# Optimization experiments

Measured on AMD Instinct MI355X. Metric: run time of the kernel, lower is better.

The kernel has to match this reference:

```python
import jax, jax.numpy as jnp
import numpy as np

H = 96          # hidden_dim / GatedGraphConv out_channels
L = 6           # num_layers
F_IN = 32       # num_node_features
G = 4096        # number of graphs in batch
BN_EPS = 1e-5


def setup_inputs() -> dict:
    key = jax.random.key(0)
    ks = jax.random.split(key, 16)
    N, E = 100000, 400000
    x = jax.random.normal(ks[0], (N, F_IN), dtype=jnp.float32)
    edge_index = jax.random.randint(ks[1], (2, E), 0, N, dtype=jnp.int64)
    batch = jnp.sort(jax.random.randint(ks[2], (N,), 0, G, dtype=jnp.int64))
    s = 1.0 / np.sqrt(H)
    conv_w = jax.random.uniform(ks[3], (L, H, H), jnp.float32, -s, s)
    w_ih = jax.random.uniform(ks[4], (3 * H, H), jnp.float32, -s, s)
    w_hh = jax.random.uniform(ks[5], (3 * H, H), jnp.float32, -s, s)
    b_ih = jax.random.uniform(ks[6], (3 * H,), jnp.float32, -s, s)
    b_hh = jax.random.uniform(ks[7], (3 * H,), jnp.float32, -s, s)
    bn_gamma = jnp.ones((H,), jnp.float32)
    bn_beta = jnp.zeros((H,), jnp.float32)
    s1 = 1.0 / np.sqrt(H)
    fc1_w = jax.random.uniform(ks[8], (4 * H, H), jnp.float32, -s1, s1)
    fc1_b = jax.random.uniform(ks[9], (4 * H,), jnp.float32, -s1, s1)
    s2 = 1.0 / np.sqrt(4 * H)
    fc2_w = jax.random.uniform(ks[10], (H, 4 * H), jnp.float32, -s2, s2)
    fc2_b = jax.random.uniform(ks[11], (H,), jnp.float32, -s2, s2)
    fc3_w = jax.random.uniform(ks[12], (1, H), jnp.float32, -s1, s1)
    fc3_b = jax.random.uniform(ks[13], (1,), jnp.float32, -s1, s1)
    return dict(x=x, edge_index=edge_index, batch=batch, conv_w=conv_w,
                w_ih=w_ih, w_hh=w_hh, b_ih=b_ih, b_hh=b_hh,
                bn_gamma=bn_gamma, bn_beta=bn_beta,
                fc1_w=fc1_w, fc1_b=fc1_b, fc2_w=fc2_w, fc2_b=fc2_b,
                fc3_w=fc3_w, fc3_b=fc3_b)


def _gated_graph_conv(x, src, dst, conv_w, w_ih, w_hh, b_ih, b_hh):
    N = x.shape[0]
    # PyG zero-pads input features up to out_channels
    h = jnp.pad(x, ((0, 0), (0, H - x.shape[1])))
    for i in range(L):
        m = h @ conv_w[i]                         # [N, H]
        agg = jnp.zeros((N, H), m.dtype).at[dst].add(m[src])  # scatter-add at targets
        gi = agg @ w_ih.T + b_ih                  # [N, 3H]
        gh = h @ w_hh.T + b_hh                    # [N, 3H]
        i_r, i_z, i_n = jnp.split(gi, 3, axis=-1)
        h_r, h_z, h_n = jnp.split(gh, 3, axis=-1)
        r = jax.nn.sigmoid(i_r + h_r)
        z = jax.nn.sigmoid(i_z + h_z)
        n = jnp.tanh(i_n + r * h_n)
        h = (1.0 - z) * n + z * h
    return h


def reference(x, edge_index, batch, conv_w, w_ih, w_hh, b_ih, b_hh,
              bn_gamma, bn_beta, fc1_w, fc1_b, fc2_w, fc2_b, fc3_w, fc3_b):
    src, dst = edge_index[0], edge_index[1]
    h = _gated_graph_conv(x, src, dst, conv_w, w_ih, w_hh, b_ih, b_hh)
    h = jax.nn.relu(h)
    # global mean pool (dropout is identity in eval)
    sums = jax.ops.segment_sum(h, batch, num_segments=G)          # [G, H]
    counts = jax.ops.segment_sum(jnp.ones((h.shape[0],), h.dtype), batch, num_segments=G)
    pooled = sums / jnp.maximum(counts, 1.0)[:, None]
    # BatchNorm1d in eval mode: running_mean=0, running_var=1
    hbn = (pooled / jnp.sqrt(1.0 + BN_EPS)) * bn_gamma + bn_beta
    h1 = jax.nn.relu(hbn @ fc1_w.T + fc1_b)
    h2 = jax.nn.relu(h1 @ fc2_w.T + fc2_b)
    return h2 @ fc3_w.T + fc3_b                                    # [G, 1]
```

## Files before the change

### kernel.cpp

```cpp
#include <hip/hip_runtime.h>

#define H96 96
#define LAYERS 6
#define BN_EPS 1e-5f
#define SCAN_B 1024

typedef unsigned short u16;
typedef unsigned int u32;
typedef _Float16 f16;
typedef _Float16 h8 __attribute__((ext_vector_type(8)));
typedef float f32x4 __attribute__((ext_vector_type(4)));
typedef u32 u32x3 __attribute__((ext_vector_type(3)));

__device__ __forceinline__ float sigm(float x) { return 1.f / (1.f + __expf(-x)); }
__device__ __forceinline__ float tanh_(float x) { return 2.f / (1.f + __expf(-2.f * x)) - 1.f; }
__device__ __forceinline__ f32x4 splat4(float x) { f32x4 v = {x, x, x, x}; return v; }
__device__ __forceinline__ h8 H8(f32x4 v) { return __builtin_bit_cast(h8, v); }

struct h2s { f16 x, y; };

__device__ __forceinline__ void upk(u32 v, float& lo, float& hi) {
    union { u32 u; h2s h; } c;
    c.u = v;
    lo = (float)c.h.x;
    hi = (float)c.h.y;
}

__global__ void k_f2h(const float* __restrict__ convw, const float* __restrict__ wih,
                      const float* __restrict__ whh, const float* __restrict__ fc1w,
                      const float* __restrict__ fc2w, f16* __restrict__ dst) {
    int i = blockIdx.x * 256 + threadIdx.x;
    if (i >= 184320) return;
    float v;
    if (i < 55296) v = convw[i];
    else if (i < 82944) v = wih[i - 55296];
    else if (i < 110592) v = whh[i - 82944];
    else if (i < 147456) v = fc1w[i - 110592];
    else v = fc2w[i - 147456];
    dst[i] = (f16)v;
}

__global__ __launch_bounds__(256) void k_wpt(const f16* __restrict__ wih16, const f16* __restrict__ convw16,
                                             f16* __restrict__ wpt) {
    int l = blockIdx.y;
    int lane = threadIdx.x & 63, wave = threadIdx.x >> 6;
    int l15 = lane & 15, q = lane >> 4;
    int rowa = blockIdx.x * 64 + wave * 16 + l15;
    if (rowa >= 288) rowa = 287;
    const f16* B = convw16 + (size_t)l * 9216;
    h8 af[3];
#pragma unroll
    for (int s = 0; s < 3; s++) af[s] = *(const h8*)(wih16 + (size_t)rowa * 96 + s * 32 + q * 8);
    f32x4 acc[6];
#pragma unroll
    for (int t = 0; t < 6; t++) acc[t] = splat4(0.f);
#pragma unroll
    for (int s = 0; s < 3; s++)
#pragma unroll
        for (int t = 0; t < 6; t++) {
            h8 b = *(const h8*)(B + (size_t)(t * 16 + l15) * 96 + s * 32 + q * 8);
            acc[t] = __builtin_amdgcn_mfma_f32_16x16x32_f16(af[s], b, acc[t], 0, 0, 0);
        }
    int rbase = blockIdx.x * 64 + wave * 16 + q * 4;
#pragma unroll
    for (int t = 0; t < 6; t++)
#pragma unroll
        for (int rr = 0; rr < 4; rr++) {
            int row = rbase + rr;
            if (row < 288) wpt[(size_t)l * 27648 + (size_t)row * 96 + t * 16 + l15] = (f16)acc[t][rr];
        }
}

__global__ void k_pad(const float* __restrict__ x, f16* __restrict__ hf, int N) {
    int i = blockIdx.x * 256 + threadIdx.x;
    if (i >= N * H96) return;
    int n = i / H96, c = i - n * H96;
    float v = (c < 32) ? x[n * 32 + c] : 0.f;
    hf[i] = (f16)v;
}

__global__ void k_hist(const int* __restrict__ key, int* __restrict__ deg, int E) {
    int e = blockIdx.x * 256 + threadIdx.x;
    if (e < E) atomicAdd(&deg[key[e]], 1);
}

__global__ __launch_bounds__(SCAN_B) void k_scan1(const int* __restrict__ deg, int* __restrict__ incl,
                                                  int* __restrict__ bsum, int N) {
    __shared__ int sh[SCAN_B];
    int i = blockIdx.x * SCAN_B + threadIdx.x;
    int v = (i < N) ? deg[i] : 0;
    sh[threadIdx.x] = v;
    __syncthreads();
    for (int off = 1; off < SCAN_B; off <<= 1) {
        int t = (threadIdx.x >= (u32)off) ? sh[threadIdx.x - off] : 0;
        __syncthreads();
        sh[threadIdx.x] += t;
        __syncthreads();
    }
    incl[blockIdx.x * SCAN_B + threadIdx.x] = sh[threadIdx.x];
    if (threadIdx.x == SCAN_B - 1) bsum[blockIdx.x] = sh[threadIdx.x];
}

__global__ void k_scan2(int* __restrict__ bsum, int nb) {
    if (blockIdx.x == 0 && threadIdx.x == 0) {
        int run = 0;
        for (int i = 0; i < nb; i++) { run += bsum[i]; bsum[i] = run; }
    }
}

__global__ void k_scan3(const int* __restrict__ deg, const int* __restrict__ incl, const int* __restrict__ bsum,
                        int* __restrict__ rs, int* __restrict__ cur, int N, int E) {
    int i = blockIdx.x * 256 + threadIdx.x;
    if (i == 0) rs[N] = E;
    if (i < N) {
        int b = i / SCAN_B;
        int off = (b > 0) ? bsum[b - 1] : 0;
        int ex = incl[i] - deg[i] + off;
        rs[i] = ex;
        if (cur) cur[i] = ex;
    }
}

__global__ void k_fill(const int* __restrict__ src, const int* __restrict__ dst, int* __restrict__ cur,
                       int* __restrict__ es, int E) {
    int e = blockIdx.x * 256 + threadIdx.x;
    if (e < E) {
        int p = atomicAdd(&cur[dst[e]], 1);
        es[p] = src[e];
    }
}

__global__ __launch_bounds__(256) void k_gather(const f16* __restrict__ hin, const int* __restrict__ rs,
                                                const int* __restrict__ es, f16* __restrict__ agg, int N) {
    int grp = threadIdx.x >> 4;
    int lane6 = threadIdx.x & 15;
    int node = blockIdx.x * 16 + grp;
    if (node >= N) return;
    int s = rs[node], e = rs[node + 1];
    float a0 = 0, a1 = 0, a2 = 0, a3 = 0, a4 = 0, a5 = 0;
    const char* basep = (const char*)hin;
    int off = lane6 * 12;
    for (int i = s; i < e; i += 4) {
        int j1 = (i + 1 < e) ? i + 1 : i;
        int j2 = (i + 2 < e) ? i + 2 : i;
        int j3 = (i + 3 < e) ? i + 3 : i;
        float m1 = (i + 1 < e) ? 1.f : 0.f;
        float m2 = (i + 2 < e) ? 1.f : 0.f;
        float m3 = (i + 3 < e) ? 1.f : 0.f;
        int sa = es[i], sb = es[j1], sc = es[j2], sd = es[j3];
        u32x3 va = *(const u32x3*)(basep + (size_t)sa * 192 + off);
        u32x3 vb = *(const u32x3*)(basep + (size_t)sb * 192 + off);
        u32x3 vc = *(const u32x3*)(basep + (size_t)sc * 192 + off);
        u32x3 vd = *(const u32x3*)(basep + (size_t)sd * 192 + off);
        float t0, t1;
        upk(va.x, t0, t1); a0 += t0; a1 += t1;
        upk(va.y, t0, t1); a2 += t0; a3 += t1;
        upk(va.z, t0, t1); a4 += t0; a5 += t1;
        upk(vb.x, t0, t1); a0 += t0 * m1; a1 += t1 * m1;
        upk(vb.y, t0, t1); a2 += t0 * m1; a3 += t1 * m1;
        upk(vb.z, t0, t1); a4 += t0 * m1; a5 += t1 * m1;
        upk(vc.x, t0, t1); a0 += t0 * m2; a1 += t1 * m2;
        upk(vc.y, t0, t1); a2 += t0 * m2; a3 += t1 * m2;
        upk(vc.z, t0, t1); a4 += t0 * m2; a5 += t1 * m2;
        upk(vd.x, t0, t1); a0 += t0 * m3; a1 += t1 * m3;
        upk(vd.y, t0, t1); a2 += t0 * m3; a3 += t1 * m3;
        upk(vd.z, t0, t1); a4 += t0 * m3; a5 += t1 * m3;
    }
    f16* dp = agg + (size_t)node * H96 + lane6 * 6;
    h2s p0, p1, p2;
    p0.x = (f16)a0; p0.y = (f16)a1;
    p1.x = (f16)a2; p1.y = (f16)a3;
    p2.x = (f16)a4; p2.y = (f16)a5;
    *(h2s*)(dp + 0) = p0;
    *(h2s*)(dp + 2) = p1;
    *(h2s*)(dp + 4) = p2;
}

__global__ __launch_bounds__(384, 2) void k_gru(const f16* __restrict__ agg, const f16* __restrict__ hin,
                                                f16* __restrict__ hout, const f16* __restrict__ wpt,
                                                const f16* __restrict__ whh, const float* __restrict__ bih,
                                                const float* __restrict__ bhh, int N) {
    int w = threadIdx.x >> 6;
    int lane = threadIdx.x & 63;
    int l15 = lane & 15, q = lane >> 4;
    int jr = w * 16 + l15;
    float b_r = bih[jr] + bhh[jr];
    float b_z = bih[96 + jr] + bhh[96 + jr];
    float b_in = bih[192 + jr];
    float b_hn = bhh[192 + jr];
    f32x4 wr0[3], wr1[3], wz0[3], wz1[3], wn0[3], wn1[3];
#pragma unroll
    for (int s = 0; s < 3; s++) {
        int ko = s * 32 + q * 8;
        wr0[s] = *(const f32x4*)(wpt + (size_t)jr * H96 + ko);
        wz0[s] = *(const f32x4*)(wpt + (size_t)(96 + jr) * H96 + ko);
        wn0[s] = *(const f32x4*)(wpt + (size_t)(192 + jr) * H96 + ko);
        wr1[s] = *(const f32x4*)(whh + (size_t)jr * H96 + ko);
        wz1[s] = *(const f32x4*)(whh + (size_t)(96 + jr) * H96 + ko);
        wn1[s] = *(const f32x4*)(whh + (size_t)(192 + jr) * H96 + ko);
    }
#pragma unroll
    for (int s = 0; s < 3; s++) {
        asm volatile("" : "+v"(wr0[s]), "+v"(wr1[s]), "+v"(wz0[s]), "+v"(wz1[s]), "+v"(wn0[s]), "+v"(wn1[s]));
    }

    int ntiles = (N + 15) >> 4;
    int stride = gridDim.x;
    int tile = blockIdx.x;
    if (tile >= ntiles) return;

    h8 as_[3], ah[3];
    {
        int rowa = (tile << 4) + l15;
        if (rowa >= N) rowa = N - 1;
#pragma unroll
        for (int s = 0; s < 3; s++) {
            as_[s] = *(const h8*)(agg + (size_t)rowa * H96 + s * 32 + q * 8);
            ah[s] = *(const h8*)(hin + (size_t)rowa * H96 + s * 32 + q * 8);
        }
    }
    while (true) {
        int nxt = tile + stride;
        int lt = (nxt < ntiles) ? nxt : tile;
        h8 as2[3], ah2[3];
        {
            int rowa = (lt << 4) + l15;
            if (rowa >= N) rowa = N - 1;
#pragma unroll
            for (int s = 0; s < 3; s++) {
                as2[s] = *(const h8*)(agg + (size_t)rowa * H96 + s * 32 + q * 8);
                ah2[s] = *(const h8*)(hin + (size_t)rowa * H96 + s * 32 + q * 8);
            }
        }
        f32x4 r = splat4(b_r), z = splat4(b_z), nn = splat4(b_in), hn = splat4(b_hn);
#pragma unroll
        for (int s = 0; s < 3; s++) {
            r = __builtin_amdgcn_mfma_f32_16x16x32_f16(as_[s], H8(wr0[s]), r, 0, 0, 0);
            r = __builtin_amdgcn_mfma_f32_16x16x32_f16(ah[s], H8(wr1[s]), r, 0, 0, 0);
            z = __builtin_amdgcn_mfma_f32_16x16x32_f16(as_[s], H8(wz0[s]), z, 0, 0, 0);
            z = __builtin_amdgcn_mfma_f32_16x16x32_f16(ah[s], H8(wz1[s]), z, 0, 0, 0);
            nn = __builtin_amdgcn_mfma_f32_16x16x32_f16(as_[s], H8(wn0[s]), nn, 0, 0, 0);
            hn = __builtin_amdgcn_mfma_f32_16x16x32_f16(ah[s], H8(wn1[s]), hn, 0, 0, 0);
        }
        int base = tile << 4;
        int rbase = base + q * 4;
#pragma unroll
        for (int rr = 0; rr < 4; rr++) {
            int row = rbase + rr;
            if (row < N) {
                float rv = sigm(r[rr]);
                float zv = sigm(z[rr]);
                float nv = tanh_(nn[rr] + rv * hn[rr]);
                size_t idx = (size_t)row * H96 + w * 16 + l15;
                float hold = (float)hin[idx];
                float hnew = (1.f - zv) * nv + zv * hold;
                hout[idx] = (f16)hnew;
            }
        }
        if (nxt >= ntiles) break;
        tile = nxt;
#pragma unroll
        for (int s = 0; s < 3; s++) {
            as_[s] = as2[s];
            ah[s] = ah2[s];
        }
    }
}

__global__ void k_pool2(const f16* __restrict__ hf, const int* __restrict__ grs,
                        const float* __restrict__ gamma, const float* __restrict__ beta,
                        f16* __restrict__ pooled, int Gn) {
    int g = blockIdx.x;
    int c = threadIdx.x;
    if (g >= Gn || c >= H96) return;
    int s = grs[g], e = grs[g + 1];
    float sum = 0.f;
    for (int n = s; n < e; n++) sum += fmaxf((float)hf[(size_t)n * H96 + c], 0.f);
    float cnt = fmaxf((float)(e - s), 1.f);
    float val = (sum / cnt) * (gamma[c] * rsqrtf(1.f + BN_EPS)) + beta[c];
    pooled[(size_t)g * H96 + c] = (f16)val;
}

template <int KS, int NT, int OUTW, bool RELU>
__global__ __launch_bounds__(256) void k_mlp(const f16* __restrict__ A, const f16* __restrict__ W,
                                             const float* __restrict__ bias, f16* __restrict__ out, int M) {
    int lane = threadIdx.x & 63, wave = threadIdx.x >> 6;
    int l15 = lane & 15, q = lane >> 4;
    int colBase = blockIdx.y * (NT * 16);
    int tile = blockIdx.x;
    int rowa = tile * 64 + wave * 16 + l15;
    if (rowa >= M) rowa = M - 1;
    h8 af[KS];
#pragma unroll
    for (int s = 0; s < KS; s++) af[s] = *(const h8*)(A + (size_t)rowa * (KS * 32) + s * 32 + q * 8);
    f32x4 acc[NT];
#pragma unroll
    for (int t = 0; t < NT; t++) acc[t] = splat4(0.f);
#pragma unroll
    for (int s = 0; s < KS; s++)
#pragma unroll
        for (int t = 0; t < NT; t++) {
            h8 b = *(const h8*)(W + (size_t)(colBase + t * 16 + l15) * (KS * 32) + s * 32 + q * 8);
            acc[t] = __builtin_amdgcn_mfma_f32_16x16x32_f16(af[s], b, acc[t], 0, 0, 0);
        }
    int rbase = tile * 64 + wave * 16 + q * 4;
#pragma unroll
    for (int t = 0; t < NT; t++) {
        float bv = bias[colBase + t * 16 + l15];
#pragma unroll
        for (int rr = 0; rr < 4; rr++) {
            int row = rbase + rr;
            if (row >= M) continue;
            float v = acc[t][rr] + bv;
            if (RELU) v = fmaxf(v, 0.f);
            out[(size_t)row * OUTW + colBase + t * 16 + l15] = (f16)v;
        }
    }
}

__global__ void k_mlp3(const f16* __restrict__ h2, const float* __restrict__ w, const float* __restrict__ b,
                       float* __restrict__ out, int M) {
    int g = blockIdx.x * 256 + threadIdx.x;
    if (g >= M) return;
    float acc = 0.f;
    for (int k = 0; k < H96; k++) acc += (float)h2[(size_t)g * H96 + k] * w[k];
    out[g] = acc + b[0];
}

extern "C" void kernel_launch(void* const* d_in, const int* in_sizes, int n_in, void* d_out, int out_size,
                              void* d_ws, size_t ws_size, hipStream_t stream) {
    const float* x = (const float*)d_in[0];
    const int* ei = (const int*)d_in[1];
    const int* batch = (const int*)d_in[2];
    const float* conv_w = (const float*)d_in[3];
    const float* wih = (const float*)d_in[4];
    const float* whh = (const float*)d_in[5];
    const float* bih = (const float*)d_in[6];
    const float* bhh = (const float*)d_in[7];
    const float* gamma = (const float*)d_in[8];
    const float* beta = (const float*)d_in[9];
    const float* fc1w = (const float*)d_in[10];
    const float* fc1b = (const float*)d_in[11];
    const float* fc2w = (const float*)d_in[12];
    const float* fc2b = (const float*)d_in[13];
    const float* fc3w = (const float*)d_in[14];
    const float* fc3b = (const float*)d_in[15];

    int N = in_sizes[0] / 32;
    int E = in_sizes[1] / 2;
    int Gn = out_size;
    const int* srcp = ei;
    const int* dstp = ei + E;

    char* p = (char*)d_ws;
    auto alloc = [&](size_t bytes) -> char* {
        char* r = p;
        p += (bytes + 255) & ~(size_t)255;
        return r;
    };
    f16* hA = (f16*)alloc((size_t)N * H96 * 2);
    f16* hB = (f16*)alloc((size_t)N * H96 * 2);
    f16* aggf = (f16*)alloc((size_t)N * H96 * 2);
    f16* wf16 = (f16*)alloc((size_t)184320 * 2);
    f16* wpt = (f16*)alloc((size_t)LAYERS * 27648 * 2);
    int nb = (N + SCAN_B - 1) / SCAN_B;
    int* deg = (int*)alloc((size_t)N * 4);
    int* incl = (int*)alloc((size_t)nb * SCAN_B * 4);
    int* bsum = (int*)alloc((size_t)nb * 4);
    int* rs = (int*)alloc((size_t)(N + 1) * 4);
    int* cur = (int*)alloc((size_t)N * 4);
    int* es = (int*)alloc((size_t)E * 4);
    int nb2 = (Gn + SCAN_B - 1) / SCAN_B;
    int* gdeg = (int*)alloc((size_t)Gn * 4);
    int* gincl = (int*)alloc((size_t)nb2 * SCAN_B * 4);
    int* gbsum = (int*)alloc((size_t)nb2 * 4);
    int* grs = (int*)alloc((size_t)(Gn + 1) * 4);
    f16* pooled = (f16*)alloc((size_t)Gn * H96 * 2);
    f16* h1 = (f16*)alloc((size_t)Gn * 384 * 2);
    f16* h2 = (f16*)alloc((size_t)Gn * H96 * 2);

    f16* convw16 = wf16;
    f16* wih16 = wf16 + 55296;
    f16* whh16 = wf16 + 82944;
    f16* fc1w16 = wf16 + 110592;
    f16* fc2w16 = wf16 + 147456;

    hipMemsetAsync(deg, 0, (size_t)N * 4, stream);
    hipMemsetAsync(gdeg, 0, (size_t)Gn * 4, stream);

    k_f2h<<<720, 256, 0, stream>>>(conv_w, wih, whh, fc1w, fc2w, wf16);
    k_wpt<<<dim3(5, 6), 256, 0, stream>>>(wih16, convw16, wpt);
    k_pad<<<(N * H96 + 255) / 256, 256, 0, stream>>>(x, hA, N);
    k_hist<<<(E + 255) / 256, 256, 0, stream>>>(dstp, deg, E);
    k_scan1<<<nb, SCAN_B, 0, stream>>>(deg, incl, bsum, N);
    k_scan2<<<1, 64, 0, stream>>>(bsum, nb);
    k_scan3<<<(N + 255) / 256, 256, 0, stream>>>(deg, incl, bsum, rs, cur, N, E);
    k_fill<<<(E + 255) / 256, 256, 0, stream>>>(srcp, dstp, cur, es, E);
    k_hist<<<(N + 255) / 256, 256, 0, stream>>>(batch, gdeg, N);
    k_scan1<<<nb2, SCAN_B, 0, stream>>>(gdeg, gincl, gbsum, Gn);
    k_scan2<<<1, 64, 0, stream>>>(gbsum, nb2);
    k_scan3<<<(Gn + 255) / 256, 256, 0, stream>>>(gdeg, gincl, gbsum, grs, (int*)nullptr, Gn, N);

    int nt16 = (N + 15) / 16;
    for (int l = 0; l < LAYERS; l++) {
        f16* hin = (l & 1) ? hB : hA;
        f16* hout = (l & 1) ? hA : hB;
        k_gather<<<nt16, 256, 0, stream>>>(hin, rs, es, aggf, N);
        k_gru<<<512, 384, 0, stream>>>(aggf, hin, hout, wpt + (size_t)l * 27648, whh16, bih, bhh, N);
    }

    k_pool2<<<Gn, 128, 0, stream>>>(hA, grs, gamma, beta, pooled, Gn);
    k_mlp<3, 6, 384, true><<<dim3((Gn + 63) / 64, 4), 256, 0, stream>>>(pooled, fc1w16, fc1b, h1, Gn);
    k_mlp<12, 6, 96, true><<<dim3((Gn + 63) / 64, 1), 256, 0, stream>>>(h1, fc2w16, fc2b, h2, Gn);
    k_mlp3<<<(Gn + 255) / 256, 256, 0, stream>>>(h2, fc3w, fc3b, (float*)d_out, Gn);
}
```

Before: 590.3 us.

## Stage GRU input tiles through double-buffered LDS and enlarge the GRU grid

In the GRU kernel, each wave used to fetch its own copy of the agg and h rows for a 16-node tile, so all six waves loaded the same rows redundantly. Now the 384 threads cooperatively load each tile once into padded, double-buffered shared memory, and every wave reads its MFMA fragments and the old h value from LDS. The grid grows from 512 to 1280 blocks to add parallelism. In exchange it adds two block barriers per tile and some LDS traffic, and the larger grid may hurt occupancy and latency hiding given the register-heavy weights.

```diff
diff --git a/kernel.cpp b/kernel.cpp
--- a/kernel.cpp
+++ b/kernel.cpp
@@ -10,6 +10,7 @@
 typedef _Float16 f16;
 typedef _Float16 h8 __attribute__((ext_vector_type(8)));
 typedef float f32x4 __attribute__((ext_vector_type(4)));
+typedef float f32x2 __attribute__((ext_vector_type(2)));
 typedef u32 u32x3 __attribute__((ext_vector_type(3)));
 
 __device__ __forceinline__ float sigm(float x) { return 1.f / (1.f + __expf(-x)); }
@@ -24,6 +25,13 @@
     c.u = v;
     lo = (float)c.h.x;
     hi = (float)c.h.y;
+}
+
+__device__ __forceinline__ h8 lds_frag(const f16* p) {
+    union { h8 v; f32x2 h[2]; } u;
+    u.h[0] = *(const f32x2*)(p);
+    u.h[1] = *(const f32x2*)(p + 4);
+    return u.v;
 }
 
 __global__ void k_f2h(const float* __restrict__ convw, const float* __restrict__ wih,
@@ -180,8 +188,12 @@
                                                 f16* __restrict__ hout, const f16* __restrict__ wpt,
                                                 const f16* __restrict__ whh, const float* __restrict__ bih,
                                                 const float* __restrict__ bhh, int N) {
-    int w = threadIdx.x >> 6;
-    int lane = threadIdx.x & 63;
+    const int TP = 100;
+    __shared__ f16 sA[2][16 * TP];
+    __shared__ f16 sH[2][16 * TP];
+    int tid = threadIdx.x;
+    int w = tid >> 6;
+    int lane = tid & 63;
     int l15 = lane & 15, q = lane >> 4;
     int jr = w * 16 + l15;
     float b_r = bih[jr] + bhh[jr];
@@ -204,33 +216,46 @@
         asm volatile("" : "+v"(wr0[s]), "+v"(wr1[s]), "+v"(wz0[s]), "+v"(wz1[s]), "+v"(wn0[s]), "+v"(wn1[s]));
     }
 
+    int mt = (tid < 192) ? tid : tid - 192;
+    int mrow = mt / 12;
+    int mcol = mt - mrow * 12;
+    const f16* smat = (tid < 192) ? agg : hin;
+    f16* sdst = (tid < 192) ? &sA[0][0] : &sH[0][0];
+    int soff = mrow * TP + mcol * 8;
+
     int ntiles = (N + 15) >> 4;
     int stride = gridDim.x;
     int tile = blockIdx.x;
     if (tile >= ntiles) return;
 
-    h8 as_[3], ah[3];
     {
-        int rowa = (tile << 4) + l15;
+        int rowa = (tile << 4) + mrow;
         if (rowa >= N) rowa = N - 1;
-#pragma unroll
-        for (int s = 0; s < 3; s++) {
-            as_[s] = *(const h8*)(agg + (size_t)rowa * H96 + s * 32 + q * 8);
-            ah[s] = *(const h8*)(hin + (size_t)rowa * H96 + s * 32 + q * 8);
-        }
-    }
+        f32x4 v = *(const f32x4*)(smat + (size_t)rowa * 96 + mcol * 8);
+        union { f32x4 v; f32x2 h[2]; } u;
+        u.v = v;
+        *(f32x2*)(sdst + soff) = u.h[0];
+        *(f32x2*)(sdst + soff + 4) = u.h[1];
+    }
+    __syncthreads();
+    int cur = 0;
     while (true) {
         int nxt = tile + stride;
-        int lt = (nxt < ntiles) ? nxt : tile;
-        h8 as2[3], ah2[3];
-        {
-            int rowa = (lt << 4) + l15;
+        bool havenext = nxt < ntiles;
+        f32x4 v2 = splat4(0.f);
+        if (havenext) {
+            int rowa = (nxt << 4) + mrow;
             if (rowa >= N) rowa = N - 1;
-#pragma unroll
-            for (int s = 0; s < 3; s++) {
-                as2[s] = *(const h8*)(agg + (size_t)rowa * H96 + s * 32 + q * 8);
-                ah2[s] = *(const h8*)(hin + (size_t)rowa * H96 + s * 32 + q * 8);
-            }
+            v2 = *(const f32x4*)(smat + (size_t)rowa * 96 + mcol * 8);
+        }
+        const f16* pA = &sA[cur][0];
+        const f16* pH = &sH[cur][0];
+        h8 as_[3], ah[3];
+#pragma unroll
+        for (int s = 0; s < 3; s++) {
+            int off = l15 * TP + s * 32 + q * 8;
+            as_[s] = lds_frag(pA + off);
+            ah[s] = lds_frag(pH + off);
         }
         f32x4 r = splat4(b_r), z = splat4(b_z), nn = splat4(b_in), hn = splat4(b_hn);
 #pragma unroll
@@ -251,19 +276,23 @@
                 float rv = sigm(r[rr]);
                 float zv = sigm(z[rr]);
                 float nv = tanh_(nn[rr] + rv * hn[rr]);
-                size_t idx = (size_t)row * H96 + w * 16 + l15;
-                float hold = (float)hin[idx];
+                float hold = (float)pH[(q * 4 + rr) * TP + w * 16 + l15];
                 float hnew = (1.f - zv) * nv + zv * hold;
-                hout[idx] = (f16)hnew;
+                hout[(size_t)row * H96 + w * 16 + l15] = (f16)hnew;
             }
         }
-        if (nxt >= ntiles) break;
+        __syncthreads();
+        if (!havenext) break;
+        {
+            union { f32x4 v; f32x2 h[2]; } u;
+            u.v = v2;
+            f16* d2 = sdst + (cur ^ 1) * (16 * TP) + soff;
+            *(f32x2*)(d2) = u.h[0];
+            *(f32x2*)(d2 + 4) = u.h[1];
+        }
+        __syncthreads();
         tile = nxt;
-#pragma unroll
-        for (int s = 0; s < 3; s++) {
-            as_[s] = as2[s];
-            ah[s] = ah2[s];
-        }
+        cur ^= 1;
     }
 }
 
@@ -406,7 +435,7 @@
         f16* hin = (l & 1) ? hB : hA;
         f16* hout = (l & 1) ? hA : hB;
         k_gather<<<nt16, 256, 0, stream>>>(hin, rs, es, aggf, N);
-        k_gru<<<512, 384, 0, stream>>>(aggf, hin, hout, wpt + (size_t)l * 27648, whh16, bih, bhh, N);
+        k_gru<<<1280, 384, 0, stream>>>(aggf, hin, hout, wpt + (size_t)l * 27648, whh16, bih, bhh, N);
     }
 
     k_pool2<<<Gn, 128, 0, stream>>>(hA, grs, gamma, beta, pooled, Gn);
```

New measurement: 610.4 us. 1.03x slower.
